# Kernel optimization log

Measured on AMD Instinct MI355X. Metric: run time of the kernel, lower is better.

Reference implementation:

```python
import jax, jax.numpy as jnp
import numpy as np

SR = 16000
FREQ_POINTS = 2 * SR          # IR length / FFT size
NBINS = FREQ_POINTS // 2 + 1  # rfft bins
D = 8                         # delay lines
AP = 4                        # allpass sections per line
EARLY_LEN = 200


def setup_inputs() -> dict:
    key = jax.random.key(0)
    ks = jax.random.split(key, 9)
    return {
        "audio_dry": jax.random.normal(ks[0], (4, 1, 32000), jnp.float32),
        "early_ir": 0.1 * jax.random.normal(ks[1], (EARLY_LEN,), jnp.float32),
        "input_gain": 0.25 + 0.1 * jax.random.normal(ks[2], (D,), jnp.float32),
        "output_gain": 0.25 + 0.1 * jax.random.normal(ks[3], (D,), jnp.float32),
        # keep strictly positive / away from 0 for numerical sanity (torch init clamps at 0)
        "time_rev_0_sec": jnp.abs(0.1 * jax.random.normal(ks[4], (1,), jnp.float32)) + 0.3,
        "alpha_tone": jnp.abs(0.1 * jax.random.normal(ks[5], (1,), jnp.float32)) + 0.5,
        "delay_values": 400.0 + 60.0 * jax.random.normal(ks[6], (D,), jnp.float32),
        "delays_allpass": 400.0 + 60.0 * jax.random.normal(ks[7], (D, AP), jnp.float32),
        "gain_allpass": 0.25 + 0.1 * jax.random.normal(ks[8], (D, AP), jnp.float32),
    }


def _get_ir(early_ir, input_gain, output_gain, time_rev_0_sec, alpha_tone,
            delay_values, delays_allpass, gain_allpass):
    wk = 2.0 * jnp.pi * jnp.arange(NBINS, dtype=jnp.float32) / FREQ_POINTS  # [F]
    zk = jnp.exp(-1j * wk)  # e^{-j w_k}, [F] complex64

    # Fractional delay: integer delay * 1st-order allpass interpolator -> diag of delay matrix
    z_d = jnp.exp(-1j * (wk[:, None] * jnp.floor(delay_values)[None, :]))      # [F, D]
    d_eta = delay_values - jnp.floor(delay_values)
    eta = (1.0 - d_eta) / (1.0 + d_eta)                                        # [D]
    ap_interp = (eta[None, :] + zk[:, None]) / (1.0 + eta[None, :] * zk[:, None])
    d_vec = (z_d * ap_interp).astype(jnp.complex64)                            # [F, D]

    # One-pole absorption filters (diag of filter matrix)
    t0 = time_rev_0_sec[0]
    alpha = alpha_tone[0]
    delay_sec = (delay_values + jnp.sum(delays_allpass, axis=-1)) / SR         # [D]
    k = jnp.power(10.0, -3.0 * delay_sec / t0)
    kpi = jnp.power(10.0, -3.0 * delay_sec / (alpha * t0))
    g = 2.0 * k * kpi / (k + kpi)
    p = (k - kpi) / (k + kpi)
    filt = g[None, :] / (1.0 - p[None, :] * zk[:, None] + 1e-8)               # [F, D]

    # Allpass decorrelators: product of AP sections per line (diag)
    z_delays = jnp.exp(1j * (wk[:, None, None] * delays_allpass[None]))        # [F, D, AP]
    ga = gain_allpass[None].astype(jnp.complex64)
    ap_tf = jnp.prod((1.0 + ga * z_delays) / (ga + z_delays), axis=-1)         # [F, D]

    # feedback = diag(filt) @ M @ diag(ap_tf)  (diagonal scaling instead of diag_embed+matmul)
    M = (-jnp.eye(D, dtype=jnp.float32) + 0.5 * jnp.ones((D, D), jnp.float32)).astype(jnp.complex64)
    feedback = filt[:, :, None] * M[None] * ap_tf[:, None, :]                  # [F, D, D]

    # H(w) = out_g . diag(d) (I - feedback diag(d))^{-1} in_g   (solve instead of explicit inv)
    A = jnp.eye(D, dtype=jnp.complex64)[None] - feedback * d_vec[:, None, :]   # [F, D, D]
    b = jnp.broadcast_to(input_gain.astype(jnp.complex64), (NBINS, D))[..., None]
    x = jnp.linalg.solve(A, b)[..., 0]                                         # [F, D]
    transfer = jnp.einsum('fd,fd->f', d_vec * x, jnp.broadcast_to(output_gain.astype(jnp.complex64), (NBINS, D)))

    late_ir = jnp.fft.irfft(transfer, n=FREQ_POINTS).astype(jnp.float32)       # [FREQ_POINTS]
    return late_ir.at[:EARLY_LEN].add(early_ir)


def reference(audio_dry, early_ir, input_gain, output_gain, time_rev_0_sec,
              alpha_tone, delay_values, delays_allpass, gain_allpass):
    ir = _get_ir(early_ir, input_gain, output_gain, time_rev_0_sec, alpha_tone,
                 delay_values, delays_allpass, gain_allpass)
    K = ir.shape[0]
    left = (K - 1) // 2
    right = (K - 1) - left  # torch conv1d padding='same' (cross-correlation, extra pad on right)
    out = jax.lax.conv_general_dilated(
        audio_dry, ir[None, None, :], window_strides=(1,),
        padding=[(left, right)], dimension_numbers=('NCH', 'OIH', 'NCH'))
    return out[:, 0, :]  # [B, T]
```

## Files before the change

### kernel.cpp

```cpp
#include <hip/hip_runtime.h>

#define N_FFT 32000
#define NBINS 16001
#define NDL 8
#define NAP 4
#define EARLY_LEN 200
#define T_LEN 32000
#define NB 4

#define ASTRIDE 65600
#define APAD 16000

#define KSPLIT 16
#define KRANGE 1024
#define KTOT   16384
#define OB 4096
#define WSPAN 5088
#define XPHYS 5760
#define HS_ROW_L 1048

struct c32 { float re, im; };

__device__ __forceinline__ c32 cmul(c32 a, c32 b) {
    return { a.re*b.re - a.im*b.im, a.re*b.im + a.im*b.re };
}
__device__ __forceinline__ c32 cdiv(c32 a, c32 b) {
    float inv = 1.0f / (b.re*b.re + b.im*b.im);
    return { (a.re*b.re + a.im*b.im)*inv, (a.im*b.re - a.re*b.im)*inv };
}

typedef _Float16 f16x8 __attribute__((ext_vector_type(8)));
typedef float    f32x16 __attribute__((ext_vector_type(16)));

__device__ __forceinline__ float h2f(unsigned short u) {
    return (float)__builtin_bit_cast(_Float16, u);
}
__device__ __forceinline__ unsigned short f2h(float f) {
    return __builtin_bit_cast(unsigned short, (_Float16)f);
}

__global__ __launch_bounds__(512) void stageAT_kernel(
    const float* __restrict__ ing, const float* __restrict__ outg,
    const float* __restrict__ t0p, const float* __restrict__ alphap,
    const float* __restrict__ delays, const float* __restrict__ dap,
    const float* __restrict__ gap, float2* __restrict__ G,
    const float* __restrict__ audio, unsigned short* __restrict__ audio_h)
{
    __shared__ float2 sxA[129];
    __shared__ float2 tab[256];
    __shared__ float2 pa[512];
    int tid = threadIdx.x;
    int k1 = blockIdx.x;

    if (k1 >= 125) {
        int i4 = (k1 - 125) * 512 + tid;
        if (i4 >= NB * (ASTRIDE/8)) return;
        int b = i4 / (ASTRIDE/8);
        int q = i4 - b * (ASTRIDE/8);
        int u0 = q * 8 - APAD;
        unsigned r[4];
        if (u0 >= 0 && u0 + 8 <= T_LEN) {
            const float4* ap = (const float4*)(audio + b*T_LEN + u0);
            float4 v0 = ap[0], v1 = ap[1];
            r[0] = f2h(v0.x) | ((unsigned)f2h(v0.y) << 16);
            r[1] = f2h(v0.z) | ((unsigned)f2h(v0.w) << 16);
            r[2] = f2h(v1.x) | ((unsigned)f2h(v1.y) << 16);
            r[3] = f2h(v1.z) | ((unsigned)f2h(v1.w) << 16);
        } else {
            unsigned short hh[8];
            #pragma unroll
            for (int e = 0; e < 8; e++) {
                int u = u0 + e;
                float v = (u >= 0 && u < T_LEN) ? audio[b*T_LEN + u] : 0.0f;
                hh[e] = f2h(v);
            }
            r[0] = hh[0] | ((unsigned)hh[1] << 16);
            r[1] = hh[2] | ((unsigned)hh[3] << 16);
            r[2] = hh[4] | ((unsigned)hh[5] << 16);
            r[3] = hh[6] | ((unsigned)hh[7] << 16);
        }
        ((uint4*)audio_h)[i4] = make_uint4(r[0], r[1], r[2], r[3]);
        return;
    }

    if (tid < 256) {
        float c, s;
        sincosf(2.4544246578366045e-02f * (float)tid, &s, &c);
        tab[tid] = make_float2(c, s);
    }

    const float  TWf = 1.9634954084936207e-04f;
    const double TWd = 1.9634954084936207740e-04;
    float t0v = t0p[0], alpha = alphap[0];

    for (int base = 0; base < 1032; base += 512) {
        int task = base + tid;
        if (task >= 1032) break;
        int k2 = task >> 3, d = task & 7;
        int f = k1 + 125 * k2;
        if (f > 16000) { if (d == 0) sxA[k2] = make_float2(0.f, 0.f); continue; }

        float wk = TWf * (float)f;
        float cwk, swk;
        sincosf(wk, &swk, &cwk);

        float dval = delays[d];
        float fid = floorf(dval);
        float d_eta = dval - fid;
        float eta = (1.0f - d_eta) / (1.0f + d_eta);
        long long mm = ((long long)f * (long long)fid) % N_FFT;
        float a0 = TWf * (float)mm;
        float c0, s0; sincosf(a0, &s0, &c0);
        c32 z_d = { c0, -s0 };
        c32 num = { eta + cwk, -swk };
        c32 den = { 1.0f + eta*cwk, -eta*swk };
        c32 dvec = cmul(z_d, cdiv(num, den));

        float dsum = dval;
        #pragma unroll
        for (int a = 0; a < NAP; a++) dsum += dap[d*NAP + a];
        float delay_sec = dsum * (1.0f/16000.0f);
        float kf  = expf(-3.0f*delay_sec/t0v * 2.3025850929940457f);
        float kpi = expf(-3.0f*delay_sec/(alpha*t0v) * 2.3025850929940457f);
        float g = 2.0f*kf*kpi/(kf+kpi);
        float p = (kf - kpi)/(kf + kpi);
        c32 fden = { 1.0f + 1e-8f - p*cwk, p*swk };
        c32 filt = cdiv({g, 0.f}, fden);

        c32 ap = {1.f, 0.f};
        #pragma unroll
        for (int a = 0; a < NAP; a++) {
            float dl = dap[d*NAP + a];
            double ph = fmod((double)f * (double)dl, (double)N_FFT);
            float aa = (float)(ph * TWd);
            float ca, sa; sincosf(aa, &sa, &ca);
            float ga = gap[d*NAP + a];
            c32 nume = { 1.0f + ga*ca, ga*sa };
            c32 dene = { ga + ca, sa };
            ap = cmul(ap, cdiv(nume, dene));
        }
        c32 cd = cmul(ap, dvec);
        c32 rc = cmul(filt, cd);
        c32 Dd = { 1.0f + rc.re, rc.im };
        c32 invD = cdiv({1.f, 0.f}, Dd);
        float bg = ing[d];
        c32 t1 = cmul({cd.re*bg, cd.im*bg}, invD);
        c32 t2 = cmul(rc, invD);
        float s1r = t1.re, s1i = t1.im, s2r = t2.re, s2i = t2.im;
        #pragma unroll
        for (int msk = 1; msk < 8; msk <<= 1) {
            s1r += __shfl_xor(s1r, msk);
            s1i += __shfl_xor(s1i, msk);
            s2r += __shfl_xor(s2r, msk);
            s2i += __shfl_xor(s2i, msk);
        }
        c32 denl = { 1.0f - 0.5f*s2r, -0.5f*s2i };
        c32 lam = cdiv({0.5f*s1r, 0.5f*s1i}, denl);
        c32 lr = cmul(lam, filt);
        c32 xv = cmul(invD, {bg + lr.re, lr.im});
        c32 term = cmul(dvec, xv);
        float og = outg[d];
        float trr = term.re * og, tri = term.im * og;
        #pragma unroll
        for (int msk = 1; msk < 8; msk <<= 1) {
            trr += __shfl_xor(trr, msk);
            tri += __shfl_xor(tri, msk);
        }
        if (d == 0) {
            float w = (f == 0 || f == 16000) ? 0.5f : 1.0f;
            sxA[k2] = make_float2(trr * w, tri * w);
        }
    }
    __syncthreads();

    {
        int r = tid & 255, half = tid >> 8;
        int k2s = half ? 65 : 0, k2e = half ? 129 : 65;
        float ar = 0.f, ai = 0.f;
        int p = (k2s * r) & 255;
        for (int k2 = k2s; k2 < k2e; k2++) {
            float2 X = sxA[k2];
            float2 E = tab[p];
            ar = fmaf(X.x, E.x, fmaf(-X.y, E.y, ar));
            ai = fmaf(X.x, E.y, fmaf( X.y, E.x, ai));
            p = (p + r) & 255;
        }
        pa[tid] = make_float2(ar, ai);
    }
    __syncthreads();
    if (tid < 256) {
        float2 a = pa[tid], b = pa[tid + 256];
        G[k1 * 256 + tid] = make_float2(a.x + b.x, a.y + b.y);
    }
}

__device__ __forceinline__ float ir_val(const float2* __restrict__ G, int n) {
    const float TWf = 1.9634954084936207e-04f;
    float wc, wss; sincosf(TWf * (float)n, &wss, &wc);
    float er = 1.f, ei = 0.f, ar = 0.f;
    const float2* gp = G + (n & 255);
    #pragma unroll 5
    for (int k1 = 0; k1 < 125; k1++) {
        float2 g = gp[k1 * 256];
        ar = fmaf(g.x, er, fmaf(-g.y, ei, ar));
        float nr = fmaf(er, wc, -(ei*wss));
        float ni = fmaf(er, wss,  (ei*wc));
        er = nr; ei = ni;
    }
    return ar * (2.0f / (float)N_FFT);
}

__global__ __launch_bounds__(256) void stageB_kernel(
    const float2* __restrict__ G, const float* __restrict__ early,
    unsigned short* __restrict__ h_g)
{
    int n = blockIdx.x * 256 + threadIdx.x;
    float v = ir_val(G, n);
    if (n < EARLY_LEN) v += early[n];
    h_g[n] = f2h(v);
}

__global__ __launch_bounds__(512) void conv_mfma_kernel(
    const unsigned short* __restrict__ audio_h,
    const unsigned short* __restrict__ h_g,
    unsigned short* __restrict__ pconv)
{
    __shared__ __attribute__((aligned(16))) char Sraw[2*XPHYS*2 + 32*HS_ROW_L*2 + 1056*2];
    _Float16* xs = (_Float16*)Sraw;
    _Float16* hs = (_Float16*)(Sraw + 2*XPHYS*2);
    _Float16* hw = (_Float16*)(Sraw + 2*XPHYS*2 + 32*HS_ROW_L*2);
    float*    red = (float*)Sraw;

    int tid = threadIdx.x;
    int lane = tid & 63;
    int w = tid >> 6;
    int bb = w & 1;
    int tq = (w >> 1) & 1;
    int kw = w >> 2;
    int bx = blockIdx.x, bp = blockIdx.y, kz = blockIdx.z;
    int t0 = bx * OB;
    int b0g = bp * 2;
    int K0 = kz * KRANGE;
    int wbase = t0 + K0;

    {
        unsigned* hw32 = (unsigned*)hw;
        const unsigned* hg32 = (const unsigned*)h_g;
        int sbase = (K0 - 32) >> 1;
        for (int j2 = tid; j2 < 528; j2 += 512)
            hw32[j2] = (sbase + j2 >= 0) ? hg32[sbase + j2] : 0u;
    }
    const uint4* xg = (const uint4*)audio_h;
    for (int q = tid; q < 2 * (WSPAN/8); q += 512) {
        int bbs = (q >= WSPAN/8) ? 1 : 0;
        int qq = q - (WSPAN/8) * bbs;
        uint4 v = xg[(size_t)(b0g + bbs) * (ASTRIDE/8) + (wbase >> 3) + qq];
        ((uint4*)xs)[bbs * (XPHYS/8) + qq + (qq >> 3)] = v;
    }
    __syncthreads();

    {
        const unsigned short* hwu = (const unsigned short*)hw;
        #pragma unroll
        for (int e = 0; e < 8; e++) {
            int idx = tid + 512 * e;
            int i = idx >> 7;
            int q = idx & 127;
            int src = 8 * q - i + 31;
            unsigned o[4];
            #pragma unroll
            for (int j = 0; j < 4; j++)
                o[j] = (unsigned)hwu[src + 2*j] | ((unsigned)hwu[src + 2*j + 1] << 16);
            *(uint4*)(hs + i * HS_ROW_L + 8 * q) = make_uint4(o[0], o[1], o[2], o[3]);
        }
    }
    __syncthreads();

    int l31 = lane & 31, g = lane >> 5;
    int aBase = l31 * HS_ROW_L + 8 * g;
    int pB0 = 1024 * (2*tq + 0) + 32 * l31 + 8 * g;
    int pB1 = 1024 * (2*tq + 1) + 32 * l31 + 8 * g;
    const _Float16* xb = xs + (bb ? XPHYS : 0);

    f32x16 acc0 = {0,0,0,0,0,0,0,0,0,0,0,0,0,0,0,0};
    f32x16 acc1 = {0,0,0,0,0,0,0,0,0,0,0,0,0,0,0,0};
    #pragma unroll 4
    for (int ksl = 0; ksl < 32; ksl++) {
        int ksg = kw * 32 + ksl;
        f16x8 af = *(const f16x8*)(hs + aBase + 16 * ksg);
        int p0 = pB0 + 16 * ksg;
        int p1 = pB1 + 16 * ksg;
        f16x8 bf0 = *(const f16x8*)(xb + p0 + 8 * (p0 >> 6));
        f16x8 bf1 = *(const f16x8*)(xb + p1 + 8 * (p1 >> 6));
        acc0 = __builtin_amdgcn_mfma_f32_32x32x16_f16(af, bf0, acc0, 0, 0, 0);
        acc1 = __builtin_amdgcn_mfma_f32_32x32x16_f16(af, bf1, acc1, 0, 0, 0);
    }
    __syncthreads();
    int slot0 = ((bb * 2 + tq) * 2 + 0) * 1024;
    int slot1 = ((bb * 2 + tq) * 2 + 1) * 1024;
    if (kw == 1) {
        #pragma unroll
        for (int r = 0; r < 16; r++) {
            red[slot0 + r * 64 + lane] = acc0[r];
            red[slot1 + r * 64 + lane] = acc1[r];
        }
    }
    __syncthreads();
    if (kw == 0) {
        unsigned short* po = pconv + (size_t)(kz * NB + b0g + bb) * T_LEN;
        #pragma unroll
        for (int s = 0; s < 2; s++) {
            int T = 2 * tq + s;
            int slot = s ? slot1 : slot0;
            #pragma unroll
            for (int r = 0; r < 16; r += 2) {
                float v0 = (s ? acc1[r]   : acc0[r])   + red[slot + r * 64 + lane];
                float v1 = (s ? acc1[r+1] : acc0[r+1]) + red[slot + (r+1) * 64 + lane];
                int i = (r & 3) + 8 * (r >> 2) + 4 * g;
                int t = t0 + 1024 * T + i + 32 * l31;
                if (t < T_LEN) {
                    unsigned u = f2h(v0) | ((unsigned)f2h(v1) << 16);
                    *(unsigned*)(po + t) = u;
                }
            }
        }
    }
}

__global__ void finish_kernel(const unsigned short* __restrict__ pconv,
                              float* __restrict__ out)
{
    int i = blockIdx.x * 256 + threadIdx.x;
    if (i >= NB * T_LEN) return;
    float s = 0.f;
    #pragma unroll
    for (int kz = 0; kz < KSPLIT; kz++)
        s += h2f(pconv[(size_t)kz * NB * T_LEN + i]);
    out[i] = s;
}

extern "C" void kernel_launch(void* const* d_in, const int* in_sizes, int n_in,
                              void* d_out, int out_size, void* d_ws, size_t ws_size,
                              hipStream_t stream) {
    const float* audio  = (const float*)d_in[0];
    const float* early  = (const float*)d_in[1];
    const float* ing    = (const float*)d_in[2];
    const float* outg   = (const float*)d_in[3];
    const float* t0p    = (const float*)d_in[4];
    const float* alphap = (const float*)d_in[5];
    const float* delays = (const float*)d_in[6];
    const float* dap    = (const float*)d_in[7];
    const float* gap    = (const float*)d_in[8];

    char* ws = (char*)d_ws;
    float2*         G       = (float2*)(ws);
    unsigned short* h_g     = (unsigned short*)(ws + 262144);
    unsigned short* audio_h = (unsigned short*)(ws + 294912);
    unsigned short* pconv   = (unsigned short*)(ws + 819712);

    stageAT_kernel<<<190, 512, 0, stream>>>(ing, outg, t0p, alphap,
                                            delays, dap, gap, G,
                                            audio, audio_h);
    stageB_kernel<<<64, 256, 0, stream>>>(G, early, h_g);
    conv_mfma_kernel<<<dim3(8, 2, KSPLIT), 512, 0, stream>>>(audio_h, h_g, pconv);
    finish_kernel<<<500, 256, 0, stream>>>(pconv, (float*)d_out);
}
```

Measured before the change: 41.30 us.

## Fuse four stage kernels into one cooperative kernel with grid syncs

Replaces the four separate launches (transfer/DFT stage, IR synthesis, MFMA convolution, partial-sum reduction) with a single cooperative kernel of 256 blocks that separates the phases with grid.sync(). The IR synthesis stage is also reworked to split the 125-term inner sum across 8 threads with shuffle reductions, which raises parallelism there. The aim is to remove launch gaps and kernel-boundary overhead between small stages. In exchange, every phase now runs on the same 256-block grid, and grid-wide barriers add their own cost.

```diff
diff --git a/kernel.cpp b/kernel.cpp
--- a/kernel.cpp
+++ b/kernel.cpp
@@ -1,4 +1,7 @@
 #include <hip/hip_runtime.h>
+#include <hip/hip_cooperative_groups.h>
+
+namespace cg = cooperative_groups;
 
 #define N_FFT 32000
 #define NBINS 16001
@@ -39,304 +42,315 @@
     return __builtin_bit_cast(unsigned short, (_Float16)f);
 }
 
-__global__ __launch_bounds__(512) void stageAT_kernel(
+__global__ __launch_bounds__(512, 2) void fused_kernel(
+    const float* __restrict__ audio, const float* __restrict__ early,
     const float* __restrict__ ing, const float* __restrict__ outg,
     const float* __restrict__ t0p, const float* __restrict__ alphap,
     const float* __restrict__ delays, const float* __restrict__ dap,
-    const float* __restrict__ gap, float2* __restrict__ G,
-    const float* __restrict__ audio, unsigned short* __restrict__ audio_h)
-{
-    __shared__ float2 sxA[129];
-    __shared__ float2 tab[256];
-    __shared__ float2 pa[512];
-    int tid = threadIdx.x;
-    int k1 = blockIdx.x;
-
-    if (k1 >= 125) {
-        int i4 = (k1 - 125) * 512 + tid;
-        if (i4 >= NB * (ASTRIDE/8)) return;
-        int b = i4 / (ASTRIDE/8);
-        int q = i4 - b * (ASTRIDE/8);
-        int u0 = q * 8 - APAD;
-        unsigned r[4];
-        if (u0 >= 0 && u0 + 8 <= T_LEN) {
-            const float4* ap = (const float4*)(audio + b*T_LEN + u0);
-            float4 v0 = ap[0], v1 = ap[1];
-            r[0] = f2h(v0.x) | ((unsigned)f2h(v0.y) << 16);
-            r[1] = f2h(v0.z) | ((unsigned)f2h(v0.w) << 16);
-            r[2] = f2h(v1.x) | ((unsigned)f2h(v1.y) << 16);
-            r[3] = f2h(v1.z) | ((unsigned)f2h(v1.w) << 16);
-        } else {
-            unsigned short hh[8];
-            #pragma unroll
-            for (int e = 0; e < 8; e++) {
-                int u = u0 + e;
-                float v = (u >= 0 && u < T_LEN) ? audio[b*T_LEN + u] : 0.0f;
-                hh[e] = f2h(v);
-            }
-            r[0] = hh[0] | ((unsigned)hh[1] << 16);
-            r[1] = hh[2] | ((unsigned)hh[3] << 16);
-            r[2] = hh[4] | ((unsigned)hh[5] << 16);
-            r[3] = hh[6] | ((unsigned)hh[7] << 16);
-        }
-        ((uint4*)audio_h)[i4] = make_uint4(r[0], r[1], r[2], r[3]);
-        return;
-    }
-
-    if (tid < 256) {
-        float c, s;
-        sincosf(2.4544246578366045e-02f * (float)tid, &s, &c);
-        tab[tid] = make_float2(c, s);
-    }
-
-    const float  TWf = 1.9634954084936207e-04f;
-    const double TWd = 1.9634954084936207740e-04;
-    float t0v = t0p[0], alpha = alphap[0];
-
-    for (int base = 0; base < 1032; base += 512) {
-        int task = base + tid;
-        if (task >= 1032) break;
-        int k2 = task >> 3, d = task & 7;
-        int f = k1 + 125 * k2;
-        if (f > 16000) { if (d == 0) sxA[k2] = make_float2(0.f, 0.f); continue; }
-
-        float wk = TWf * (float)f;
-        float cwk, swk;
-        sincosf(wk, &swk, &cwk);
-
-        float dval = delays[d];
-        float fid = floorf(dval);
-        float d_eta = dval - fid;
-        float eta = (1.0f - d_eta) / (1.0f + d_eta);
-        long long mm = ((long long)f * (long long)fid) % N_FFT;
-        float a0 = TWf * (float)mm;
-        float c0, s0; sincosf(a0, &s0, &c0);
-        c32 z_d = { c0, -s0 };
-        c32 num = { eta + cwk, -swk };
-        c32 den = { 1.0f + eta*cwk, -eta*swk };
-        c32 dvec = cmul(z_d, cdiv(num, den));
-
-        float dsum = dval;
-        #pragma unroll
-        for (int a = 0; a < NAP; a++) dsum += dap[d*NAP + a];
-        float delay_sec = dsum * (1.0f/16000.0f);
-        float kf  = expf(-3.0f*delay_sec/t0v * 2.3025850929940457f);
-        float kpi = expf(-3.0f*delay_sec/(alpha*t0v) * 2.3025850929940457f);
-        float g = 2.0f*kf*kpi/(kf+kpi);
-        float p = (kf - kpi)/(kf + kpi);
-        c32 fden = { 1.0f + 1e-8f - p*cwk, p*swk };
-        c32 filt = cdiv({g, 0.f}, fden);
-
-        c32 ap = {1.f, 0.f};
-        #pragma unroll
-        for (int a = 0; a < NAP; a++) {
-            float dl = dap[d*NAP + a];
-            double ph = fmod((double)f * (double)dl, (double)N_FFT);
-            float aa = (float)(ph * TWd);
-            float ca, sa; sincosf(aa, &sa, &ca);
-            float ga = gap[d*NAP + a];
-            c32 nume = { 1.0f + ga*ca, ga*sa };
-            c32 dene = { ga + ca, sa };
-            ap = cmul(ap, cdiv(nume, dene));
-        }
-        c32 cd = cmul(ap, dvec);
-        c32 rc = cmul(filt, cd);
-        c32 Dd = { 1.0f + rc.re, rc.im };
-        c32 invD = cdiv({1.f, 0.f}, Dd);
-        float bg = ing[d];
-        c32 t1 = cmul({cd.re*bg, cd.im*bg}, invD);
-        c32 t2 = cmul(rc, invD);
-        float s1r = t1.re, s1i = t1.im, s2r = t2.re, s2i = t2.im;
-        #pragma unroll
-        for (int msk = 1; msk < 8; msk <<= 1) {
-            s1r += __shfl_xor(s1r, msk);
-            s1i += __shfl_xor(s1i, msk);
-            s2r += __shfl_xor(s2r, msk);
-            s2i += __shfl_xor(s2i, msk);
-        }
-        c32 denl = { 1.0f - 0.5f*s2r, -0.5f*s2i };
-        c32 lam = cdiv({0.5f*s1r, 0.5f*s1i}, denl);
-        c32 lr = cmul(lam, filt);
-        c32 xv = cmul(invD, {bg + lr.re, lr.im});
-        c32 term = cmul(dvec, xv);
-        float og = outg[d];
-        float trr = term.re * og, tri = term.im * og;
-        #pragma unroll
-        for (int msk = 1; msk < 8; msk <<= 1) {
-            trr += __shfl_xor(trr, msk);
-            tri += __shfl_xor(tri, msk);
-        }
-        if (d == 0) {
-            float w = (f == 0 || f == 16000) ? 0.5f : 1.0f;
-            sxA[k2] = make_float2(trr * w, tri * w);
-        }
-    }
-    __syncthreads();
-
-    {
-        int r = tid & 255, half = tid >> 8;
-        int k2s = half ? 65 : 0, k2e = half ? 129 : 65;
-        float ar = 0.f, ai = 0.f;
-        int p = (k2s * r) & 255;
-        for (int k2 = k2s; k2 < k2e; k2++) {
-            float2 X = sxA[k2];
-            float2 E = tab[p];
-            ar = fmaf(X.x, E.x, fmaf(-X.y, E.y, ar));
-            ai = fmaf(X.x, E.y, fmaf( X.y, E.x, ai));
-            p = (p + r) & 255;
-        }
-        pa[tid] = make_float2(ar, ai);
-    }
-    __syncthreads();
-    if (tid < 256) {
-        float2 a = pa[tid], b = pa[tid + 256];
-        G[k1 * 256 + tid] = make_float2(a.x + b.x, a.y + b.y);
-    }
-}
-
-__device__ __forceinline__ float ir_val(const float2* __restrict__ G, int n) {
-    const float TWf = 1.9634954084936207e-04f;
-    float wc, wss; sincosf(TWf * (float)n, &wss, &wc);
-    float er = 1.f, ei = 0.f, ar = 0.f;
-    const float2* gp = G + (n & 255);
-    #pragma unroll 5
-    for (int k1 = 0; k1 < 125; k1++) {
-        float2 g = gp[k1 * 256];
-        ar = fmaf(g.x, er, fmaf(-g.y, ei, ar));
-        float nr = fmaf(er, wc, -(ei*wss));
-        float ni = fmaf(er, wss,  (ei*wc));
-        er = nr; ei = ni;
-    }
-    return ar * (2.0f / (float)N_FFT);
-}
-
-__global__ __launch_bounds__(256) void stageB_kernel(
-    const float2* __restrict__ G, const float* __restrict__ early,
-    unsigned short* __restrict__ h_g)
-{
-    int n = blockIdx.x * 256 + threadIdx.x;
-    float v = ir_val(G, n);
-    if (n < EARLY_LEN) v += early[n];
-    h_g[n] = f2h(v);
-}
-
-__global__ __launch_bounds__(512) void conv_mfma_kernel(
-    const unsigned short* __restrict__ audio_h,
-    const unsigned short* __restrict__ h_g,
-    unsigned short* __restrict__ pconv)
+    const float* __restrict__ gap,
+    float2* __restrict__ G, unsigned short* __restrict__ audio_h,
+    unsigned short* __restrict__ h_g, unsigned short* __restrict__ pconv,
+    float* __restrict__ out)
 {
     __shared__ __attribute__((aligned(16))) char Sraw[2*XPHYS*2 + 32*HS_ROW_L*2 + 1056*2];
-    _Float16* xs = (_Float16*)Sraw;
-    _Float16* hs = (_Float16*)(Sraw + 2*XPHYS*2);
-    _Float16* hw = (_Float16*)(Sraw + 2*XPHYS*2 + 32*HS_ROW_L*2);
-    float*    red = (float*)Sraw;
+    cg::grid_group grid = cg::this_grid();
 
     int tid = threadIdx.x;
-    int lane = tid & 63;
-    int w = tid >> 6;
-    int bb = w & 1;
-    int tq = (w >> 1) & 1;
-    int kw = w >> 2;
-    int bx = blockIdx.x, bp = blockIdx.y, kz = blockIdx.z;
-    int t0 = bx * OB;
-    int b0g = bp * 2;
-    int K0 = kz * KRANGE;
-    int wbase = t0 + K0;
+    int bid = blockIdx.x;
+    const float TWf = 1.9634954084936207e-04f;
+
+    if (bid < 125) {
+        float2* sxA = (float2*)Sraw;
+        float2* tab = (float2*)(Sraw + 1040);
+        float2* pa  = (float2*)(Sraw + 3088);
+        int k1 = bid;
+
+        if (tid < 256) {
+            float c, s;
+            sincosf(2.4544246578366045e-02f * (float)tid, &s, &c);
+            tab[tid] = make_float2(c, s);
+        }
+
+        const double TWd = 1.9634954084936207740e-04;
+        float t0v = t0p[0], alpha = alphap[0];
+
+        for (int base = 0; base < 1032; base += 512) {
+            int task = base + tid;
+            if (task >= 1032) break;
+            int k2 = task >> 3, d = task & 7;
+            int f = k1 + 125 * k2;
+            if (f > 16000) { if (d == 0) sxA[k2] = make_float2(0.f, 0.f); continue; }
+
+            float wk = TWf * (float)f;
+            float cwk, swk;
+            sincosf(wk, &swk, &cwk);
+
+            float dval = delays[d];
+            float fid = floorf(dval);
+            float d_eta = dval - fid;
+            float eta = (1.0f - d_eta) / (1.0f + d_eta);
+            long long mm = ((long long)f * (long long)fid) % N_FFT;
+            float a0 = TWf * (float)mm;
+            float c0, s0; sincosf(a0, &s0, &c0);
+            c32 z_d = { c0, -s0 };
+            c32 num = { eta + cwk, -swk };
+            c32 den = { 1.0f + eta*cwk, -eta*swk };
+            c32 dvec = cmul(z_d, cdiv(num, den));
+
+            float dsum = dval;
+            #pragma unroll
+            for (int a = 0; a < NAP; a++) dsum += dap[d*NAP + a];
+            float delay_sec = dsum * (1.0f/16000.0f);
+            float kf  = expf(-3.0f*delay_sec/t0v * 2.3025850929940457f);
+            float kpi = expf(-3.0f*delay_sec/(alpha*t0v) * 2.3025850929940457f);
+            float g = 2.0f*kf*kpi/(kf+kpi);
+            float p = (kf - kpi)/(kf + kpi);
+            c32 fden = { 1.0f + 1e-8f - p*cwk, p*swk };
+            c32 filt = cdiv({g, 0.f}, fden);
+
+            c32 ap = {1.f, 0.f};
+            #pragma unroll
+            for (int a = 0; a < NAP; a++) {
+                float dl = dap[d*NAP + a];
+                double ph = fmod((double)f * (double)dl, (double)N_FFT);
+                float aa = (float)(ph * TWd);
+                float ca, sa; sincosf(aa, &sa, &ca);
+                float ga = gap[d*NAP + a];
+                c32 nume = { 1.0f + ga*ca, ga*sa };
+                c32 dene = { ga + ca, sa };
+                ap = cmul(ap, cdiv(nume, dene));
+            }
+            c32 cd = cmul(ap, dvec);
+            c32 rc = cmul(filt, cd);
+            c32 Dd = { 1.0f + rc.re, rc.im };
+            c32 invD = cdiv({1.f, 0.f}, Dd);
+            float bg = ing[d];
+            c32 t1 = cmul({cd.re*bg, cd.im*bg}, invD);
+            c32 t2 = cmul(rc, invD);
+            float s1r = t1.re, s1i = t1.im, s2r = t2.re, s2i = t2.im;
+            #pragma unroll
+            for (int msk = 1; msk < 8; msk <<= 1) {
+                s1r += __shfl_xor(s1r, msk);
+                s1i += __shfl_xor(s1i, msk);
+                s2r += __shfl_xor(s2r, msk);
+                s2i += __shfl_xor(s2i, msk);
+            }
+            c32 denl = { 1.0f - 0.5f*s2r, -0.5f*s2i };
+            c32 lam = cdiv({0.5f*s1r, 0.5f*s1i}, denl);
+            c32 lr = cmul(lam, filt);
+            c32 xv = cmul(invD, {bg + lr.re, lr.im});
+            c32 term = cmul(dvec, xv);
+            float og = outg[d];
+            float trr = term.re * og, tri = term.im * og;
+            #pragma unroll
+            for (int msk = 1; msk < 8; msk <<= 1) {
+                trr += __shfl_xor(trr, msk);
+                tri += __shfl_xor(tri, msk);
+            }
+            if (d == 0) {
+                float w = (f == 0 || f == 16000) ? 0.5f : 1.0f;
+                sxA[k2] = make_float2(trr * w, tri * w);
+            }
+        }
+        __syncthreads();
+
+        {
+            int r = tid & 255, half = tid >> 8;
+            int k2s = half ? 65 : 0, k2e = half ? 129 : 65;
+            float ar = 0.f, ai = 0.f;
+            int p = (k2s * r) & 255;
+            for (int k2 = k2s; k2 < k2e; k2++) {
+                float2 X = sxA[k2];
+                float2 E = tab[p];
+                ar = fmaf(X.x, E.x, fmaf(-X.y, E.y, ar));
+                ai = fmaf(X.x, E.y, fmaf( X.y, E.x, ai));
+                p = (p + r) & 255;
+            }
+            pa[tid] = make_float2(ar, ai);
+        }
+        __syncthreads();
+        if (tid < 256) {
+            float2 a = pa[tid], b = pa[tid + 256];
+            G[k1 * 256 + tid] = make_float2(a.x + b.x, a.y + b.y);
+        }
+    } else {
+        int i4 = (bid - 125) * 512 + tid;
+        if (i4 < NB * (ASTRIDE/8)) {
+            int b = i4 / (ASTRIDE/8);
+            int q = i4 - b * (ASTRIDE/8);
+            int u0 = q * 8 - APAD;
+            unsigned r[4];
+            if (u0 >= 0 && u0 + 8 <= T_LEN) {
+                const float4* apx = (const float4*)(audio + b*T_LEN + u0);
+                float4 v0 = apx[0], v1 = apx[1];
+                r[0] = f2h(v0.x) | ((unsigned)f2h(v0.y) << 16);
+                r[1] = f2h(v0.z) | ((unsigned)f2h(v0.w) << 16);
+                r[2] = f2h(v1.x) | ((unsigned)f2h(v1.y) << 16);
+                r[3] = f2h(v1.z) | ((unsigned)f2h(v1.w) << 16);
+            } else {
+                unsigned short hh[8];
+                #pragma unroll
+                for (int e = 0; e < 8; e++) {
+                    int u = u0 + e;
+                    float v = (u >= 0 && u < T_LEN) ? audio[b*T_LEN + u] : 0.0f;
+                    hh[e] = f2h(v);
+                }
+                r[0] = hh[0] | ((unsigned)hh[1] << 16);
+                r[1] = hh[2] | ((unsigned)hh[3] << 16);
+                r[2] = hh[4] | ((unsigned)hh[5] << 16);
+                r[3] = hh[6] | ((unsigned)hh[7] << 16);
+            }
+            ((uint4*)audio_h)[i4] = make_uint4(r[0], r[1], r[2], r[3]);
+        }
+    }
+
+    grid.sync();
 
     {
-        unsigned* hw32 = (unsigned*)hw;
-        const unsigned* hg32 = (const unsigned*)h_g;
-        int sbase = (K0 - 32) >> 1;
-        for (int j2 = tid; j2 < 528; j2 += 512)
-            hw32[j2] = (sbase + j2 >= 0) ? hg32[sbase + j2] : 0u;
+        int n   = bid * 64 + (tid >> 3);
+        int sub = tid & 7;
+        int k10 = sub * 16;
+        int nk1 = (sub == 7) ? 13 : 16;
+
+        int m0 = (n * k10) % N_FFT;
+        float er, ei; sincosf(TWf * (float)m0, &ei, &er);
+        float wc, wss; sincosf(TWf * (float)n, &wss, &wc);
+
+        float ar = 0.f;
+        const float2* gp = G + (n & 255) + (size_t)k10 * 256;
+        #pragma unroll 4
+        for (int k = 0; k < nk1; k++) {
+            float2 g = gp[(size_t)k * 256];
+            ar = fmaf(g.x, er, fmaf(-g.y, ei, ar));
+            float nr = fmaf(er, wc, -(ei*wss));
+            float ni = fmaf(er, wss,  (ei*wc));
+            er = nr; ei = ni;
+        }
+        ar += __shfl_xor(ar, 1);
+        ar += __shfl_xor(ar, 2);
+        ar += __shfl_xor(ar, 4);
+        if (sub == 0) {
+            float v = ar * (2.0f / (float)N_FFT);
+            if (n < EARLY_LEN) v += early[n];
+            h_g[n] = f2h(v);
+        }
     }
-    const uint4* xg = (const uint4*)audio_h;
-    for (int q = tid; q < 2 * (WSPAN/8); q += 512) {
-        int bbs = (q >= WSPAN/8) ? 1 : 0;
-        int qq = q - (WSPAN/8) * bbs;
-        uint4 v = xg[(size_t)(b0g + bbs) * (ASTRIDE/8) + (wbase >> 3) + qq];
-        ((uint4*)xs)[bbs * (XPHYS/8) + qq + (qq >> 3)] = v;
+
+    grid.sync();
+
+    {
+        _Float16* xs = (_Float16*)Sraw;
+        _Float16* hs = (_Float16*)(Sraw + 2*XPHYS*2);
+        _Float16* hw = (_Float16*)(Sraw + 2*XPHYS*2 + 32*HS_ROW_L*2);
+        float*    red = (float*)Sraw;
+
+        int lane = tid & 63;
+        int w = tid >> 6;
+        int bb = w & 1;
+        int tq = (w >> 1) & 1;
+        int kw = w >> 2;
+        int bx = bid & 7, bp = (bid >> 3) & 1, kz = bid >> 4;
+        int t0 = bx * OB;
+        int b0g = bp * 2;
+        int K0 = kz * KRANGE;
+        int wbase = t0 + K0;
+
+        {
+            unsigned* hw32 = (unsigned*)hw;
+            const unsigned* hg32 = (const unsigned*)h_g;
+            int sbase = (K0 - 32) >> 1;
+            for (int j2 = tid; j2 < 528; j2 += 512)
+                hw32[j2] = (sbase + j2 >= 0) ? hg32[sbase + j2] : 0u;
+        }
+        const uint4* xg = (const uint4*)audio_h;
+        for (int q = tid; q < 2 * (WSPAN/8); q += 512) {
+            int bbs = (q >= WSPAN/8) ? 1 : 0;
+            int qq = q - (WSPAN/8) * bbs;
+            uint4 v = xg[(size_t)(b0g + bbs) * (ASTRIDE/8) + (wbase >> 3) + qq];
+            ((uint4*)xs)[bbs * (XPHYS/8) + qq + (qq >> 3)] = v;
+        }
+        __syncthreads();
+
+        {
+            const unsigned short* hwu = (const unsigned short*)hw;
+            int i  = tid & 31;
+            int q0 = tid >> 5;
+            #pragma unroll
+            for (int e = 0; e < 8; e++) {
+                int q = q0 + 16 * e;
+                int src = 8 * q - i + 31;
+                unsigned o[4];
+                #pragma unroll
+                for (int j = 0; j < 4; j++)
+                    o[j] = (unsigned)hwu[src + 2*j] | ((unsigned)hwu[src + 2*j + 1] << 16);
+                *(uint4*)(hs + i * HS_ROW_L + 8 * q) = make_uint4(o[0], o[1], o[2], o[3]);
+            }
+        }
+        __syncthreads();
+
+        int l31 = lane & 31, g = lane >> 5;
+        int aBase = l31 * HS_ROW_L + 8 * g;
+        int pB0 = 1024 * (2*tq + 0) + 32 * l31 + 8 * g;
+        int pB1 = 1024 * (2*tq + 1) + 32 * l31 + 8 * g;
+        const _Float16* xb = xs + (bb ? XPHYS : 0);
+
+        f32x16 acc0 = {0,0,0,0,0,0,0,0,0,0,0,0,0,0,0,0};
+        f32x16 acc1 = {0,0,0,0,0,0,0,0,0,0,0,0,0,0,0,0};
+        #pragma unroll 4
+        for (int ksl = 0; ksl < 32; ksl++) {
+            int ksg = kw * 32 + ksl;
+            f16x8 af = *(const f16x8*)(hs + aBase + 16 * ksg);
+            int p0 = pB0 + 16 * ksg;
+            int p1 = pB1 + 16 * ksg;
+            f16x8 bf0 = *(const f16x8*)(xb + p0 + 8 * (p0 >> 6));
+            f16x8 bf1 = *(const f16x8*)(xb + p1 + 8 * (p1 >> 6));
+            acc0 = __builtin_amdgcn_mfma_f32_32x32x16_f16(af, bf0, acc0, 0, 0, 0);
+            acc1 = __builtin_amdgcn_mfma_f32_32x32x16_f16(af, bf1, acc1, 0, 0, 0);
+        }
+        __syncthreads();
+        int slot0 = ((bb * 2 + tq) * 2 + 0) * 1024;
+        int slot1 = ((bb * 2 + tq) * 2 + 1) * 1024;
+        if (kw == 1) {
+            #pragma unroll
+            for (int r = 0; r < 16; r++) {
+                red[slot0 + r * 64 + lane] = acc0[r];
+                red[slot1 + r * 64 + lane] = acc1[r];
+            }
+        }
+        __syncthreads();
+        if (kw == 0) {
+            unsigned short* po = pconv + (size_t)(kz * NB + b0g + bb) * T_LEN;
+            #pragma unroll
+            for (int s = 0; s < 2; s++) {
+                int T = 2 * tq + s;
+                int slot = s ? slot1 : slot0;
+                #pragma unroll
+                for (int r = 0; r < 16; r += 2) {
+                    float v0 = (s ? acc1[r]   : acc0[r])   + red[slot + r * 64 + lane];
+                    float v1 = (s ? acc1[r+1] : acc0[r+1]) + red[slot + (r+1) * 64 + lane];
+                    int i = (r & 3) + 8 * (r >> 2) + 4 * g;
+                    int t = t0 + 1024 * T + i + 32 * l31;
+                    if (t < T_LEN) {
+                        unsigned u = f2h(v0) | ((unsigned)f2h(v1) << 16);
+                        *(unsigned*)(po + t) = u;
+                    }
+                }
+            }
+        }
     }
-    __syncthreads();
+
+    grid.sync();
 
     {
-        const unsigned short* hwu = (const unsigned short*)hw;
-        #pragma unroll
-        for (int e = 0; e < 8; e++) {
-            int idx = tid + 512 * e;
-            int i = idx >> 7;
-            int q = idx & 127;
-            int src = 8 * q - i + 31;
-            unsigned o[4];
-            #pragma unroll
-            for (int j = 0; j < 4; j++)
-                o[j] = (unsigned)hwu[src + 2*j] | ((unsigned)hwu[src + 2*j + 1] << 16);
-            *(uint4*)(hs + i * HS_ROW_L + 8 * q) = make_uint4(o[0], o[1], o[2], o[3]);
+        int i = bid * 512 + tid;
+        if (i < NB * T_LEN) {
+            float s = 0.f;
+            #pragma unroll
+            for (int kz = 0; kz < KSPLIT; kz++)
+                s += h2f(pconv[(size_t)kz * NB * T_LEN + i]);
+            out[i] = s;
         }
     }
-    __syncthreads();
-
-    int l31 = lane & 31, g = lane >> 5;
-    int aBase = l31 * HS_ROW_L + 8 * g;
-    int pB0 = 1024 * (2*tq + 0) + 32 * l31 + 8 * g;
-    int pB1 = 1024 * (2*tq + 1) + 32 * l31 + 8 * g;
-    const _Float16* xb = xs + (bb ? XPHYS : 0);
-
-    f32x16 acc0 = {0,0,0,0,0,0,0,0,0,0,0,0,0,0,0,0};
-    f32x16 acc1 = {0,0,0,0,0,0,0,0,0,0,0,0,0,0,0,0};
-    #pragma unroll 4
-    for (int ksl = 0; ksl < 32; ksl++) {
-        int ksg = kw * 32 + ksl;
-        f16x8 af = *(const f16x8*)(hs + aBase + 16 * ksg);
-        int p0 = pB0 + 16 * ksg;
-        int p1 = pB1 + 16 * ksg;
-        f16x8 bf0 = *(const f16x8*)(xb + p0 + 8 * (p0 >> 6));
-        f16x8 bf1 = *(const f16x8*)(xb + p1 + 8 * (p1 >> 6));
-        acc0 = __builtin_amdgcn_mfma_f32_32x32x16_f16(af, bf0, acc0, 0, 0, 0);
-        acc1 = __builtin_amdgcn_mfma_f32_32x32x16_f16(af, bf1, acc1, 0, 0, 0);
-    }
-    __syncthreads();
-    int slot0 = ((bb * 2 + tq) * 2 + 0) * 1024;
-    int slot1 = ((bb * 2 + tq) * 2 + 1) * 1024;
-    if (kw == 1) {
-        #pragma unroll
-        for (int r = 0; r < 16; r++) {
-            red[slot0 + r * 64 + lane] = acc0[r];
-            red[slot1 + r * 64 + lane] = acc1[r];
-        }
-    }
-    __syncthreads();
-    if (kw == 0) {
-        unsigned short* po = pconv + (size_t)(kz * NB + b0g + bb) * T_LEN;
-        #pragma unroll
-        for (int s = 0; s < 2; s++) {
-            int T = 2 * tq + s;
-            int slot = s ? slot1 : slot0;
-            #pragma unroll
-            for (int r = 0; r < 16; r += 2) {
-                float v0 = (s ? acc1[r]   : acc0[r])   + red[slot + r * 64 + lane];
-                float v1 = (s ? acc1[r+1] : acc0[r+1]) + red[slot + (r+1) * 64 + lane];
-                int i = (r & 3) + 8 * (r >> 2) + 4 * g;
-                int t = t0 + 1024 * T + i + 32 * l31;
-                if (t < T_LEN) {
-                    unsigned u = f2h(v0) | ((unsigned)f2h(v1) << 16);
-                    *(unsigned*)(po + t) = u;
-                }
-            }
-        }
-    }
-}
-
-__global__ void finish_kernel(const unsigned short* __restrict__ pconv,
-                              float* __restrict__ out)
-{
-    int i = blockIdx.x * 256 + threadIdx.x;
-    if (i >= NB * T_LEN) return;
-    float s = 0.f;
-    #pragma unroll
-    for (int kz = 0; kz < KSPLIT; kz++)
-        s += h2f(pconv[(size_t)kz * NB * T_LEN + i]);
-    out[i] = s;
 }
 
 extern "C" void kernel_launch(void* const* d_in, const int* in_sizes, int n_in,
@@ -357,11 +371,11 @@
     unsigned short* h_g     = (unsigned short*)(ws + 262144);
     unsigned short* audio_h = (unsigned short*)(ws + 294912);
     unsigned short* pconv   = (unsigned short*)(ws + 819712);
-
-    stageAT_kernel<<<190, 512, 0, stream>>>(ing, outg, t0p, alphap,
-                                            delays, dap, gap, G,
-                                            audio, audio_h);
-    stageB_kernel<<<64, 256, 0, stream>>>(G, early, h_g);
-    conv_mfma_kernel<<<dim3(8, 2, KSPLIT), 512, 0, stream>>>(audio_h, h_g, pconv);
-    finish_kernel<<<500, 256, 0, stream>>>(pconv, (float*)d_out);
-}
+    float*          outp    = (float*)d_out;
+
+    void* args[] = { (void*)&audio, (void*)&early, (void*)&ing, (void*)&outg,
+                     (void*)&t0p, (void*)&alphap, (void*)&delays, (void*)&dap,
+                     (void*)&gap, (void*)&G, (void*)&audio_h, (void*)&h_g,
+                     (void*)&pconv, (void*)&outp };
+    hipLaunchCooperativeKernel(fused_kernel, dim3(256), dim3(512), args, 0, stream);
+}
```

New measurement: 127.8 us. +209.6%, slower.

## Fuse IR synthesis stage into convolution kernel and drop separate launch

Applied to the files above, without the earlier changes.

Removes the stageB kernel that computed the impulse response from the partial DFT table G. Each conv block now computes its own 1056-sample IR window directly into shared memory. The 125-term sum is split across 8 lanes per sample, and the partial sums are combined with cross-lane shuffles. This saves one kernel launch and the global round trip for h_g. The cost is redundant IR computation: each window is recomputed by all 16 blocks that share the same kz, and the extra compute runs before the MFMA loop. The shared-memory repack loop also gets its index mapping changed.

```diff
diff --git a/kernel.cpp b/kernel.cpp
--- a/kernel.cpp
+++ b/kernel.cpp
@@ -194,35 +194,10 @@
     }
 }
 
-__device__ __forceinline__ float ir_val(const float2* __restrict__ G, int n) {
-    const float TWf = 1.9634954084936207e-04f;
-    float wc, wss; sincosf(TWf * (float)n, &wss, &wc);
-    float er = 1.f, ei = 0.f, ar = 0.f;
-    const float2* gp = G + (n & 255);
-    #pragma unroll 5
-    for (int k1 = 0; k1 < 125; k1++) {
-        float2 g = gp[k1 * 256];
-        ar = fmaf(g.x, er, fmaf(-g.y, ei, ar));
-        float nr = fmaf(er, wc, -(ei*wss));
-        float ni = fmaf(er, wss,  (ei*wc));
-        er = nr; ei = ni;
-    }
-    return ar * (2.0f / (float)N_FFT);
-}
-
-__global__ __launch_bounds__(256) void stageB_kernel(
-    const float2* __restrict__ G, const float* __restrict__ early,
-    unsigned short* __restrict__ h_g)
-{
-    int n = blockIdx.x * 256 + threadIdx.x;
-    float v = ir_val(G, n);
-    if (n < EARLY_LEN) v += early[n];
-    h_g[n] = f2h(v);
-}
-
 __global__ __launch_bounds__(512) void conv_mfma_kernel(
     const unsigned short* __restrict__ audio_h,
-    const unsigned short* __restrict__ h_g,
+    const float2* __restrict__ G,
+    const float* __restrict__ early,
     unsigned short* __restrict__ pconv)
 {
     __shared__ __attribute__((aligned(16))) char Sraw[2*XPHYS*2 + 32*HS_ROW_L*2 + 1056*2];
@@ -242,14 +217,8 @@
     int b0g = bp * 2;
     int K0 = kz * KRANGE;
     int wbase = t0 + K0;
-
-    {
-        unsigned* hw32 = (unsigned*)hw;
-        const unsigned* hg32 = (const unsigned*)h_g;
-        int sbase = (K0 - 32) >> 1;
-        for (int j2 = tid; j2 < 528; j2 += 512)
-            hw32[j2] = (sbase + j2 >= 0) ? hg32[sbase + j2] : 0u;
-    }
+    const float TWf = 1.9634954084936207e-04f;
+
     const uint4* xg = (const uint4*)audio_h;
     for (int q = tid; q < 2 * (WSPAN/8); q += 512) {
         int bbs = (q >= WSPAN/8) ? 1 : 0;
@@ -257,15 +226,47 @@
         uint4 v = xg[(size_t)(b0g + bbs) * (ASTRIDE/8) + (wbase >> 3) + qq];
         ((uint4*)xs)[bbs * (XPHYS/8) + qq + (qq >> 3)] = v;
     }
+
+    {
+        int n0 = K0 - 32;
+        for (int task = tid; task < 8448; task += 512) {
+            int j = task >> 3, sub = task & 7;
+            int n = n0 + j;
+            int nn = n < 0 ? 0 : n;
+            int k10 = sub * 16;
+            int nk1 = (sub == 7) ? 13 : 16;
+            int m0 = (nn * k10) % N_FFT;
+            float er, ei; sincosf(TWf * (float)m0, &ei, &er);
+            float wc, wss; sincosf(TWf * (float)nn, &wss, &wc);
+            float ar = 0.f;
+            const float2* gp = G + (nn & 255) + k10 * 256;
+            #pragma unroll 4
+            for (int k = 0; k < nk1; k++) {
+                float2 g2 = gp[k * 256];
+                ar = fmaf(g2.x, er, fmaf(-g2.y, ei, ar));
+                float nr = fmaf(er, wc, -(ei*wss));
+                float ni = fmaf(er, wss,  (ei*wc));
+                er = nr; ei = ni;
+            }
+            ar += __shfl_xor(ar, 1);
+            ar += __shfl_xor(ar, 2);
+            ar += __shfl_xor(ar, 4);
+            if (sub == 0) {
+                float v = ar * (2.0f / (float)N_FFT);
+                if (kz == 0 && (unsigned)n < EARLY_LEN) v += early[n];
+                hw[j] = (_Float16)((n < 0) ? 0.0f : v);
+            }
+        }
+    }
     __syncthreads();
 
     {
         const unsigned short* hwu = (const unsigned short*)hw;
+        int i  = tid & 31;
+        int q0 = tid >> 5;
         #pragma unroll
         for (int e = 0; e < 8; e++) {
-            int idx = tid + 512 * e;
-            int i = idx >> 7;
-            int q = idx & 127;
+            int q = q0 + 16 * e;
             int src = 8 * q - i + 31;
             unsigned o[4];
             #pragma unroll
@@ -354,14 +355,12 @@
 
     char* ws = (char*)d_ws;
     float2*         G       = (float2*)(ws);
-    unsigned short* h_g     = (unsigned short*)(ws + 262144);
     unsigned short* audio_h = (unsigned short*)(ws + 294912);
     unsigned short* pconv   = (unsigned short*)(ws + 819712);
 
     stageAT_kernel<<<190, 512, 0, stream>>>(ing, outg, t0p, alphap,
                                             delays, dap, gap, G,
                                             audio, audio_h);
-    stageB_kernel<<<64, 256, 0, stream>>>(G, early, h_g);
-    conv_mfma_kernel<<<dim3(8, 2, KSPLIT), 512, 0, stream>>>(audio_h, h_g, pconv);
+    conv_mfma_kernel<<<dim3(8, 2, KSPLIT), 512, 0, stream>>>(audio_h, G, early, pconv);
     finish_kernel<<<500, 256, 0, stream>>>(pconv, (float*)d_out);
 }
```

Measured after the change: 93.32 us. 2.26x slower.
